# Performance work log

Measured on AMD Instinct MI355X. Metric: run time of the kernel, lower is better.

Reference implementation:

```python
import jax, jax.numpy as jnp
import numpy as np

CODEBOOK_SIZE = 1024
EMBEDDING_DIM = 256
COMMITMENT_COST = 0.25


def setup_inputs() -> dict:
    key = jax.random.key(0)
    k1, k2 = jax.random.split(key)
    x = jax.random.normal(k1, (32, EMBEDDING_DIM, 32, 32), dtype=jnp.float32)
    # embedding initialized uniform(-1/K, 1/K) like the torch module
    embedding = jax.random.uniform(
        k2, (CODEBOOK_SIZE, EMBEDDING_DIM), dtype=jnp.float32,
        minval=-1.0 / CODEBOOK_SIZE, maxval=1.0 / CODEBOOK_SIZE)
    return {"x": x, "embedding": embedding}


def reference(x, embedding):
    # x: [B, C, H, W] -> inputs: [B, H, W, C]
    inputs = jnp.transpose(x, (0, 2, 3, 1))
    input_shape = inputs.shape
    flat = inputs.reshape(-1, EMBEDDING_DIM)  # [N, D]
    # squared L2 distances to codebook: [N, K]
    distances = (jnp.sum(flat ** 2, axis=1, keepdims=True)
                 + jnp.sum(embedding ** 2, axis=1)
                 - 2.0 * flat @ embedding.T)
    encoding_indices = jnp.argmin(distances, axis=1)  # [N]
    encodings = jax.nn.one_hot(encoding_indices, CODEBOOK_SIZE, dtype=jnp.float32)  # [N, K]
    # gather (same math as encodings @ embedding)
    quantized = embedding[encoding_indices].reshape(input_shape)  # [B, H, W, C]
    e_latent_loss = jnp.mean((jax.lax.stop_gradient(quantized) - inputs) ** 2)
    q_latent_loss = jnp.mean((quantized - jax.lax.stop_gradient(inputs)) ** 2)
    loss = q_latent_loss + COMMITMENT_COST * e_latent_loss
    # straight-through estimator
    quantized_st = inputs + jax.lax.stop_gradient(quantized - inputs)
    return (loss, jnp.transpose(quantized_st, (0, 3, 1, 2)), encodings)
```

## Files before the change

kernel.cpp:

```cpp
#include <hip/hip_runtime.h>
#include <cstdint>
#include <cstddef>

constexpr int B = 32, C = 256, H = 32, W = 32;
constexpr int NPTS = B * H * W;
constexpr int DIM  = 256;
constexpr int K    = 1024;
constexpr int QELEMS = B * C * H * W;
constexpr int CHW = C * H * W;

typedef __attribute__((ext_vector_type(8))) short s8v;
typedef __attribute__((ext_vector_type(4))) float f32x4;

#define GLD_LDS16(g, l)                                                        \
  __builtin_amdgcn_global_load_lds(                                            \
      (const __attribute__((address_space(1))) unsigned int*)(g),              \
      (__attribute__((address_space(3))) unsigned int*)(l), 16, 0, 0)

__device__ __forceinline__ unsigned short f2bf(float f) {
  unsigned u = __float_as_uint(f);
  return (unsigned short)((u + 0x7FFFu + ((u >> 16) & 1u)) >> 16);
}

__global__ __launch_bounds__(256) void prep_kernel(
    const float* __restrict__ x, const float* __restrict__ emb,
    unsigned short* __restrict__ ehi, float* __restrict__ esq,
    unsigned short* __restrict__ xhi, float* __restrict__ xsq,
    float* __restrict__ loss) {
  __shared__ float xls[DIM][64];
  const int t = threadIdx.x;

  if (blockIdx.x < 16) {
    if (blockIdx.x == 0 && t == 0) *loss = 0.f;
    float (*sums)[64] = (float (*)[64])xls;
    const int k = blockIdx.x * 64 + (t & 63);
    const int seg = t >> 6;
    const float* er = emb + (size_t)k * DIM + seg * 64;
    float v[64];
    float4* v4 = (float4*)v;
#pragma unroll
    for (int i = 0; i < 16; ++i) v4[i] = *(const float4*)(er + i * 4);
    float s = 0.f;
#pragma unroll
    for (int i = 0; i < 64; ++i) s = fmaf(v[i], v[i], s);
    unsigned short* eo = ehi + (size_t)k * DIM + seg * 64;
#pragma unroll
    for (int i = 0; i < 8; ++i) {
      unsigned short h[8];
#pragma unroll
      for (int j = 0; j < 8; ++j) h[j] = f2bf(v[i * 8 + j]);
      *(s8v*)(eo + i * 8) = *(s8v*)h;
    }
    sums[seg][t & 63] = s;
    __syncthreads();
    if (t < 64)
      esq[blockIdx.x * 64 + t] =
          ((sums[0][t] + sums[1][t]) + sums[2][t]) + sums[3][t];
    return;
  }

  const int n0 = (blockIdx.x - 16) * 64;
  const int bb = n0 >> 10, hw0 = n0 & 1023;
  const int p = t & 63, cs = t >> 6;
  const float* xb = x + (size_t)bb * CHW + hw0;
#pragma unroll 8
  for (int r = 0; r < 64; ++r) {
    const int c = r * 4 + cs;
    xls[c][p] = xb[(size_t)c * 1024 + p];
  }
  __syncthreads();
  if (t < 64) {
    float s = 0.f;
#pragma unroll 8
    for (int c = 0; c < 256; ++c) {
      const float v = xls[c][t];
      s = fmaf(v, v, s);
    }
    xsq[n0 + t] = s;
  }
  const int p2 = t >> 2, cb = (t & 3) * 64;
  unsigned short* xo = xhi + (size_t)(n0 + p2) * DIM + cb;
#pragma unroll
  for (int i = 0; i < 8; ++i) {
    unsigned short h[8];
#pragma unroll
    for (int j = 0; j < 8; ++j) h[j] = f2bf(xls[cb + i * 8 + j][p2]);
    *(s8v*)(xo + i * 8) = *(s8v*)h;
  }
}

constexpr float MARGIN = 1e-3f;
__global__ __launch_bounds__(256) void coarse_kernel(
    const unsigned short* __restrict__ xhi, const unsigned short* __restrict__ ehi,
    const float* __restrict__ esq, const float* __restrict__ xsq,
    float* __restrict__ part, unsigned int* __restrict__ cand) {
  __shared__ __align__(16) unsigned short xs[128][32];
  __shared__ __align__(16) unsigned short es[128][32];
  __shared__ float xsq_s[128], esq_s[128], thr_s[128];
  __shared__ unsigned long long red2[2][128];
  __shared__ unsigned int cntL[128];

  const int t = threadIdx.x;
  const int lane = t & 63, w = t >> 6;
  const int wn = (w & 1) * 64, wk = (w >> 1) * 64;
  const int col = lane & 15, quad = lane >> 4;
  const int nblk = blockIdx.x * 128;
  const int kblk = blockIdx.y * 128;

  if (t < 128) {
    xsq_s[t] = xsq[nblk + t];
    esq_s[t] = esq[kblk + t];
    cntL[t] = 0u;
  }

  f32x4 acc[4][4];
#pragma unroll
  for (int i = 0; i < 4; ++i)
#pragma unroll
    for (int j = 0; j < 4; ++j) acc[i][j] = (f32x4){0.f, 0.f, 0.f, 0.f};

  const int gl_row = lane >> 2;
  const int gl_c   = (lane & 3) * 8;

  for (int c0 = 0; c0 < DIM; c0 += 32) {
    __syncthreads();
#pragma unroll
    for (int i = 0; i < 2; ++i) {
      const int inst = w + 4 * i;
      const int row = inst * 16 + gl_row;
      GLD_LDS16(xhi + (size_t)(nblk + row) * DIM + c0 + gl_c, &xs[inst * 16][0]);
      GLD_LDS16(ehi + (size_t)(kblk + row) * DIM + c0 + gl_c, &es[inst * 16][0]);
    }
    __syncthreads();
    s8v a[4], b[4];
#pragma unroll
    for (int ti = 0; ti < 4; ++ti)
      a[ti] = *(const s8v*)&xs[wn + ti * 16 + col][quad * 8];
#pragma unroll
    for (int tj = 0; tj < 4; ++tj)
      b[tj] = *(const s8v*)&es[wk + tj * 16 + col][quad * 8];
#pragma unroll
    for (int ti = 0; ti < 4; ++ti)
#pragma unroll
      for (int tj = 0; tj < 4; ++tj)
        acc[ti][tj] = __builtin_amdgcn_mfma_f32_16x16x32_bf16(
            a[ti], b[tj], acc[ti][tj], 0, 0, 0);
  }

  unsigned long long nmin[4][4];
#pragma unroll
  for (int ti = 0; ti < 4; ++ti)
#pragma unroll
    for (int r = 0; r < 4; ++r) nmin[ti][r] = ~0ULL;
#pragma unroll
  for (int ti = 0; ti < 4; ++ti)
#pragma unroll
    for (int tj = 0; tj < 4; ++tj) {
      const int krel = wk + tj * 16 + col;
      const float eq = esq_s[krel];
#pragma unroll
      for (int r = 0; r < 4; ++r) {
        const int nl = wn + ti * 16 + quad * 4 + r;
        const float d = (xsq_s[nl] + eq) - 2.f * acc[ti][tj][r];
        const unsigned long long key =
            ((unsigned long long)__float_as_uint(d) << 32) |
            (unsigned)(kblk + krel);
        if (key < nmin[ti][r]) nmin[ti][r] = key;
      }
    }
#pragma unroll
  for (int o = 1; o < 16; o <<= 1)
#pragma unroll
    for (int ti = 0; ti < 4; ++ti)
#pragma unroll
      for (int r = 0; r < 4; ++r) {
        const unsigned long long v = __shfl_xor(nmin[ti][r], o, 64);
        if (v < nmin[ti][r]) nmin[ti][r] = v;
      }
  if (col == 0) {
#pragma unroll
    for (int ti = 0; ti < 4; ++ti)
#pragma unroll
      for (int r = 0; r < 4; ++r)
        red2[w >> 1][wn + ti * 16 + quad * 4 + r] = nmin[ti][r];
  }
  __syncthreads();
  if (t < 128) {
    const unsigned long long m0 = red2[0][t], m1 = red2[1][t];
    const unsigned long long m = (m1 < m0) ? m1 : m0;
    const float dmin = __uint_as_float((unsigned)(m >> 32));
    part[(size_t)(nblk + t) * 8 + blockIdx.y] = dmin;
    thr_s[t] = dmin + MARGIN;
  }
  __syncthreads();
#pragma unroll
  for (int ti = 0; ti < 4; ++ti)
#pragma unroll
    for (int tj = 0; tj < 4; ++tj) {
      const int krel = wk + tj * 16 + col;
      const float eq = esq_s[krel];
#pragma unroll
      for (int r = 0; r < 4; ++r) {
        const int nl = wn + ti * 16 + quad * 4 + r;
        const float d = (xsq_s[nl] + eq) - 2.f * acc[ti][tj][r];
        if (d <= thr_s[nl]) {
          const unsigned slot = atomicAdd(&cntL[nl], 1u);
          if (slot < 4u)
            cand[((size_t)(nblk + nl) * 8 + blockIdx.y) * 4 + slot] =
                (unsigned)(kblk + krel);
        }
      }
    }
  __syncthreads();
  if (t < 128) {
    unsigned c = cntL[t];
    const size_t base = ((size_t)(nblk + t) * 8 + blockIdx.y) * 4;
    if (c > 4u) { cand[base + 3] = 0xFFFFFFFEu; c = 3u; }
    for (unsigned s = c; s < 4u; ++s) cand[base + s] = 0xFFFFFFFFu;
  }
}

__global__ __launch_bounds__(256) void finish_kernel(
    const float* __restrict__ x, const float* __restrict__ emb,
    const float* __restrict__ esq, const float* __restrict__ xsq,
    const float* __restrict__ part, const unsigned int* __restrict__ cand,
    float* __restrict__ outq, float* __restrict__ enc,
    float* __restrict__ loss) {
  __shared__ __align__(16) float xls[DIM][32];
  __shared__ __align__(16) char smem2[16640];
  unsigned* list            = (unsigned*)smem2;
  unsigned long long* best  = (unsigned long long*)(smem2 + 4096);
  float* thr_s              = (float*)(smem2 + 4352);
  float* xsq_s              = (float*)(smem2 + 4480);
  int* lcnt                 = (int*)(smem2 + 4608);
  float (*tile)[16]         = (float (*)[16])smem2;
  int* ids                  = (int*)(smem2 + 16384);
  float* lred               = (float*)(smem2 + 16512);

  const int t = threadIdx.x;
  const int n0 = blockIdx.x * 32;
  const int bb = n0 >> 10, hw0 = n0 & 1023;

  const float* xb = x + (size_t)bb * CHW + hw0;
  {
    const int p = t & 31, cs = t >> 5;
#pragma unroll 8
    for (int r = 0; r < 32; ++r) {
      const int c = r * 8 + cs;
      xls[c][p] = xb[(size_t)c * 1024 + p];
    }
  }
  if (t == 0) *lcnt = 0;
  if (t < 32) {
    best[t] = ~0ULL;
    xsq_s[t] = xsq[n0 + t];
    const float4 p0 = *(const float4*)&part[(size_t)(n0 + t) * 8];
    const float4 p1 = *(const float4*)&part[(size_t)(n0 + t) * 8 + 4];
    float g = fminf(fminf(fminf(p0.x, p0.y), fminf(p0.z, p0.w)),
                    fminf(fminf(p1.x, p1.y), fminf(p1.z, p1.w)));
    thr_s[t] = g + MARGIN;
  }
  __syncthreads();

  {
    const int nn = t >> 3, s = t & 7;
    const float pv = part[(size_t)(n0 + nn) * 8 + s];
    if (pv <= thr_s[nn]) {
      const uint4 c4 = *(const uint4*)&cand[((size_t)(n0 + nn) * 8 + s) * 4];
      const unsigned vs[4] = {c4.x, c4.y, c4.z, c4.w};
#pragma unroll
      for (int i = 0; i < 4; ++i) {
        const unsigned v = vs[i];
        if (v == 0xFFFFFFFFu) continue;
        const unsigned entry = (v == 0xFFFFFFFEu)
                                   ? ((unsigned)nn << 11) | 1024u | (unsigned)s
                                   : ((unsigned)nn << 11) | (v & 1023u);
        const int pos = atomicAdd(lcnt, 1);
        if (pos < 1024) list[pos] = entry;
      }
    }
  }
  __syncthreads();

  const int L = *lcnt < 1024 ? *lcnt : 1024;
  for (int e = t; e < L; e += 256) {
    const unsigned entry = list[e];
    const int p = entry >> 11;
    const float xq = xsq_s[p];
    int klo, khi;
    if (entry & 1024u) { const int s = entry & 7; klo = s * 128; khi = klo + 128; }
    else               { klo = entry & 1023u; khi = klo + 1; }
    for (int k = klo; k < khi; ++k) {
      const float* er = emb + (size_t)k * DIM;
      float dot = 0.f;
#pragma unroll 4
      for (int c4 = 0; c4 < DIM; c4 += 4) {
        const float4 e4 = *(const float4*)(er + c4);
        dot = fmaf(xls[c4 + 0][p], e4.x, dot);
        dot = fmaf(xls[c4 + 1][p], e4.y, dot);
        dot = fmaf(xls[c4 + 2][p], e4.z, dot);
        dot = fmaf(xls[c4 + 3][p], e4.w, dot);
      }
      const float t1 = xq + esq[k];
      const float d = t1 - 2.f * dot;
      const unsigned long long key =
          ((unsigned long long)__float_as_uint(d) << 32) | (unsigned)k;
      atomicMin(&best[p], key);
    }
  }
  __syncthreads();
  if (t < 32) ids[t] = (int)(best[t] & 0xFFFFFFFFu);
  __syncthreads();

  float lsum = 0.f;
  float* ob = outq + (size_t)bb * CHW + hw0;
#pragma unroll
  for (int h = 0; h < 2; ++h) {
    const int p16 = t & 15, cs16 = t >> 4;
    const int row = ids[h * 16 + p16];
    const float* er = emb + (size_t)row * DIM + cs16 * 16;
#pragma unroll
    for (int i = 0; i < 4; ++i) {
      const float4 v = *(const float4*)(er + i * 4);
      const int c = cs16 * 16 + i * 4;
      tile[c + 0][p16] = v.x;
      tile[c + 1][p16] = v.y;
      tile[c + 2][p16] = v.z;
      tile[c + 3][p16] = v.w;
    }
    __syncthreads();
#pragma unroll
    for (int i = 0; i < 16; ++i) {
      const int c = cs16 + i * 16;
      const float q  = tile[c][p16];
      const float xv = xls[c][h * 16 + p16];
      ob[(size_t)c * 1024 + h * 16 + p16] = q;
      const float d = q - xv;
      lsum = fmaf(d, d, lsum);
    }
    __syncthreads();
  }
  float s = lsum;
#pragma unroll
  for (int o = 32; o > 0; o >>= 1) s += __shfl_down(s, o, 64);
  if ((t & 63) == 0) lred[t >> 6] = s;

  if (t < 255) {
    const int kb = 3 + 4 * t;
#pragma unroll 4
    for (int r = 0; r < 32; ++r) {
      const int id = ids[r];
      float4 v = {0.f, 0.f, 0.f, 0.f};
      const unsigned rel = (unsigned)(id - kb);
      if (rel < 4u) ((float*)&v)[rel] = 1.f;
      *(float4*)(enc + (size_t)(n0 + r) * K + kb) = v;
    }
  } else {
    for (int r = 0; r < 32; ++r) {
      const int id = ids[r];
      float* eb = enc + (size_t)(n0 + r) * K;
      eb[0] = (id == 0) ? 1.f : 0.f;
      eb[1] = (id == 1) ? 1.f : 0.f;
      eb[2] = (id == 2) ? 1.f : 0.f;
      eb[1023] = (id == 1023) ? 1.f : 0.f;
    }
  }

  __syncthreads();
  if (t == 0) {
    const float tot = (lred[0] + lred[1] + lred[2] + lred[3]) * (1.25f / (float)QELEMS);
    atomicAdd(loss, tot);
  }
}

extern "C" void kernel_launch(void* const* d_in, const int* in_sizes, int n_in,
                              void* d_out, int out_size, void* d_ws, size_t ws_size,
                              hipStream_t stream) {
  const float* x   = (const float*)d_in[0];
  const float* emb = (const float*)d_in[1];
  float* out  = (float*)d_out;
  float* loss = out;
  float* outq = out + 1;
  float* enc  = out + 1 + QELEMS;

  char* ws = (char*)d_ws;
  unsigned short* ehi  = (unsigned short*)ws;
  float*          esq  = (float*)(ws + 524288);
  float*          xsq  = (float*)(ws + 528384);
  float*          part = (float*)(ws + 659456);
  unsigned int*   cand = (unsigned int*)(ws + 1708032);
  unsigned short* xhi  = (unsigned short*)(ws + 5902336);

  prep_kernel<<<16 + NPTS / 64, 256, 0, stream>>>(x, emb, ehi, esq, xhi, xsq,
                                                  loss);
  dim3 cg(NPTS / 128, 8);
  coarse_kernel<<<cg, 256, 0, stream>>>(xhi, ehi, esq, xsq, part, cand);
  finish_kernel<<<NPTS / 32, 256, 0, stream>>>(x, emb, esq, xsq, part, cand,
                                               outq, enc, loss);
}
```

Measured before the change: 288.3 us.

## Zero encodings in coarse kernel, scatter ones in finish, halve finish tile

The dense zero-fill of the 128MB one-hot encodings moves into the coarse kernel, where each of its blocks writes one 64KB slice after the MFMA loop so the stores can overlap compute-heavy work. The finish kernel then writes only a single 1.0 per point. The finish kernel also handles 16 points per block instead of 32, uses a padded x tile, and writes quantized output straight from registers without the transpose staging tile. The risks are a correctness dependency on the zero-fill finishing before finish writes its ones (the same-stream ordering guarantees this) and extra store pressure inside coarse.

```diff
diff --git a/kernel.cpp b/kernel.cpp
--- a/kernel.cpp
+++ b/kernel.cpp
@@ -93,7 +93,8 @@
 __global__ __launch_bounds__(256) void coarse_kernel(
     const unsigned short* __restrict__ xhi, const unsigned short* __restrict__ ehi,
     const float* __restrict__ esq, const float* __restrict__ xsq,
-    float* __restrict__ part, unsigned int* __restrict__ cand) {
+    float* __restrict__ part, unsigned int* __restrict__ cand,
+    float* __restrict__ encz) {
   __shared__ __align__(16) unsigned short xs[128][32];
   __shared__ __align__(16) unsigned short es[128][32];
   __shared__ float xsq_s[128], esq_s[128], thr_s[128];
@@ -145,6 +146,19 @@
       for (int tj = 0; tj < 4; ++tj)
         acc[ti][tj] = __builtin_amdgcn_mfma_f32_16x16x32_bf16(
             a[ti], b[tj], acc[ti][tj], 0, 0, 0);
+  }
+
+  {
+    const size_t bidx = (size_t)blockIdx.y * gridDim.x + blockIdx.x;
+    float* sl = encz + bidx * 16384;
+    float4* b4 = (float4*)(sl + 3);
+    const float4 z4 = {0.f, 0.f, 0.f, 0.f};
+#pragma unroll
+    for (int j = 0; j < 16; ++j) {
+      const int idx = t + j * 256;
+      if (idx < 4095) b4[idx] = z4;
+    }
+    if (t == 0) { sl[0] = 0.f; sl[1] = 0.f; sl[2] = 0.f; sl[16383] = 0.f; }
   }
 
   unsigned long long nmin[4][4];
@@ -226,32 +240,30 @@
     const float* __restrict__ part, const unsigned int* __restrict__ cand,
     float* __restrict__ outq, float* __restrict__ enc,
     float* __restrict__ loss) {
-  __shared__ __align__(16) float xls[DIM][32];
-  __shared__ __align__(16) char smem2[16640];
-  unsigned* list            = (unsigned*)smem2;
-  unsigned long long* best  = (unsigned long long*)(smem2 + 4096);
-  float* thr_s              = (float*)(smem2 + 4352);
-  float* xsq_s              = (float*)(smem2 + 4480);
-  int* lcnt                 = (int*)(smem2 + 4608);
-  float (*tile)[16]         = (float (*)[16])smem2;
-  int* ids                  = (int*)(smem2 + 16384);
-  float* lred               = (float*)(smem2 + 16512);
+  __shared__ __align__(16) float xls[DIM][17];
+  __shared__ unsigned list[512];
+  __shared__ unsigned long long best[16];
+  __shared__ float thr_s[16];
+  __shared__ float xsq_s[16];
+  __shared__ float lred[4];
+  __shared__ int ids[16];
+  __shared__ int lcnt;
 
   const int t = threadIdx.x;
-  const int n0 = blockIdx.x * 32;
+  const int n0 = blockIdx.x * 16;
   const int bb = n0 >> 10, hw0 = n0 & 1023;
 
   const float* xb = x + (size_t)bb * CHW + hw0;
   {
-    const int p = t & 31, cs = t >> 5;
-#pragma unroll 8
-    for (int r = 0; r < 32; ++r) {
-      const int c = r * 8 + cs;
+    const int p = t & 15, cs = t >> 4;
+#pragma unroll 4
+    for (int r = 0; r < 16; ++r) {
+      const int c = r * 16 + cs;
       xls[c][p] = xb[(size_t)c * 1024 + p];
     }
   }
-  if (t == 0) *lcnt = 0;
-  if (t < 32) {
+  if (t == 0) lcnt = 0;
+  if (t < 16) {
     best[t] = ~0ULL;
     xsq_s[t] = xsq[n0 + t];
     const float4 p0 = *(const float4*)&part[(size_t)(n0 + t) * 8];
@@ -262,7 +274,7 @@
   }
   __syncthreads();
 
-  {
+  if (t < 128) {
     const int nn = t >> 3, s = t & 7;
     const float pv = part[(size_t)(n0 + nn) * 8 + s];
     if (pv <= thr_s[nn]) {
@@ -275,14 +287,14 @@
         const unsigned entry = (v == 0xFFFFFFFEu)
                                    ? ((unsigned)nn << 11) | 1024u | (unsigned)s
                                    : ((unsigned)nn << 11) | (v & 1023u);
-        const int pos = atomicAdd(lcnt, 1);
-        if (pos < 1024) list[pos] = entry;
-      }
-    }
-  }
-  __syncthreads();
-
-  const int L = *lcnt < 1024 ? *lcnt : 1024;
+        const int pos = atomicAdd(&lcnt, 1);
+        if (pos < 512) list[pos] = entry;
+      }
+    }
+  }
+  __syncthreads();
+
+  const int L = lcnt < 512 ? lcnt : 512;
   for (int e = t; e < L; e += 256) {
     const unsigned entry = list[e];
     const int p = entry >> 11;
@@ -309,66 +321,44 @@
     }
   }
   __syncthreads();
-  if (t < 32) ids[t] = (int)(best[t] & 0xFFFFFFFFu);
+  if (t < 16) ids[t] = (int)(best[t] & 0xFFFFFFFFu);
   __syncthreads();
 
   float lsum = 0.f;
-  float* ob = outq + (size_t)bb * CHW + hw0;
-#pragma unroll
-  for (int h = 0; h < 2; ++h) {
-    const int p16 = t & 15, cs16 = t >> 4;
-    const int row = ids[h * 16 + p16];
-    const float* er = emb + (size_t)row * DIM + cs16 * 16;
+  {
+    const int p = t & 15, g = t >> 4;
+    const int row = ids[p];
+    const float* er = emb + (size_t)row * DIM + g * 16;
+    float* ob = outq + (size_t)bb * CHW + hw0 + p;
 #pragma unroll
     for (int i = 0; i < 4; ++i) {
       const float4 v = *(const float4*)(er + i * 4);
-      const int c = cs16 * 16 + i * 4;
-      tile[c + 0][p16] = v.x;
-      tile[c + 1][p16] = v.y;
-      tile[c + 2][p16] = v.z;
-      tile[c + 3][p16] = v.w;
-    }
-    __syncthreads();
-#pragma unroll
-    for (int i = 0; i < 16; ++i) {
-      const int c = cs16 + i * 16;
-      const float q  = tile[c][p16];
-      const float xv = xls[c][h * 16 + p16];
-      ob[(size_t)c * 1024 + h * 16 + p16] = q;
-      const float d = q - xv;
-      lsum = fmaf(d, d, lsum);
-    }
-    __syncthreads();
-  }
+      const int c = g * 16 + i * 4;
+      float d0 = v.x - xls[c + 0][p];
+      float d1 = v.y - xls[c + 1][p];
+      float d2 = v.z - xls[c + 2][p];
+      float d3 = v.w - xls[c + 3][p];
+      ob[(size_t)(c + 0) * 1024] = v.x;
+      ob[(size_t)(c + 1) * 1024] = v.y;
+      ob[(size_t)(c + 2) * 1024] = v.z;
+      ob[(size_t)(c + 3) * 1024] = v.w;
+      lsum = fmaf(d0, d0, lsum);
+      lsum = fmaf(d1, d1, lsum);
+      lsum = fmaf(d2, d2, lsum);
+      lsum = fmaf(d3, d3, lsum);
+    }
+  }
+
+  if (t < 16) enc[(size_t)(n0 + t) * K + ids[t]] = 1.0f;
+
   float s = lsum;
 #pragma unroll
   for (int o = 32; o > 0; o >>= 1) s += __shfl_down(s, o, 64);
   if ((t & 63) == 0) lred[t >> 6] = s;
-
-  if (t < 255) {
-    const int kb = 3 + 4 * t;
-#pragma unroll 4
-    for (int r = 0; r < 32; ++r) {
-      const int id = ids[r];
-      float4 v = {0.f, 0.f, 0.f, 0.f};
-      const unsigned rel = (unsigned)(id - kb);
-      if (rel < 4u) ((float*)&v)[rel] = 1.f;
-      *(float4*)(enc + (size_t)(n0 + r) * K + kb) = v;
-    }
-  } else {
-    for (int r = 0; r < 32; ++r) {
-      const int id = ids[r];
-      float* eb = enc + (size_t)(n0 + r) * K;
-      eb[0] = (id == 0) ? 1.f : 0.f;
-      eb[1] = (id == 1) ? 1.f : 0.f;
-      eb[2] = (id == 2) ? 1.f : 0.f;
-      eb[1023] = (id == 1023) ? 1.f : 0.f;
-    }
-  }
-
   __syncthreads();
   if (t == 0) {
-    const float tot = (lred[0] + lred[1] + lred[2] + lred[3]) * (1.25f / (float)QELEMS);
+    const float tot = (((lred[0] + lred[1]) + lred[2]) + lred[3]) *
+                      (1.25f / (float)QELEMS);
     atomicAdd(loss, tot);
   }
 }
@@ -394,7 +384,7 @@
   prep_kernel<<<16 + NPTS / 64, 256, 0, stream>>>(x, emb, ehi, esq, xhi, xsq,
                                                   loss);
   dim3 cg(NPTS / 128, 8);
-  coarse_kernel<<<cg, 256, 0, stream>>>(xhi, ehi, esq, xsq, part, cand);
-  finish_kernel<<<NPTS / 32, 256, 0, stream>>>(x, emb, esq, xsq, part, cand,
+  coarse_kernel<<<cg, 256, 0, stream>>>(xhi, ehi, esq, xsq, part, cand, enc);
+  finish_kernel<<<NPTS / 16, 256, 0, stream>>>(x, emb, esq, xsq, part, cand,
                                                outq, enc, loss);
 }
```

Measured after the change: 287.8 us. No clear change (-0.2%).
